# Kernel tuning notes

Measured on AMD Instinct MI355X. Metric: run time of the kernel, lower is better.

## Reference

```python
import jax, jax.numpy as jnp
import numpy as np

B, N, E = 2, 2048, 1024
H = 16
D = E // H  # head dim = 64


def setup_inputs() -> dict:
    key = jax.random.key(0)
    ks = jax.random.split(key, 11)
    s = 1.0 / np.sqrt(E)
    return {
        "q": jax.random.normal(ks[0], (B, N, E), jnp.float32),
        "k": jax.random.normal(ks[1], (B, N, E), jnp.float32),
        "v": jax.random.normal(ks[2], (B, N, E), jnp.float32),
        "Wq": jax.random.normal(ks[3], (E, E), jnp.float32) * s,
        "bq": jnp.zeros((E,), jnp.float32),
        "Wk": jax.random.normal(ks[4], (E, E), jnp.float32) * s,
        "bk": jnp.zeros((E,), jnp.float32),
        "Wv": jax.random.normal(ks[5], (E, E), jnp.float32) * s,
        "bv": jnp.zeros((E,), jnp.float32),
        "Wo": jax.random.normal(ks[6], (E, E), jnp.float32) * s,
        "bo": jnp.zeros((E,), jnp.float32),
    }


def reference(q, k, v, Wq, bq, Wk, bk, Wv, bv, Wo, bo):
    # projections (torch Linear: x @ W^T + b)
    qp = q @ Wq.T + bq  # [B,N,E]
    kp = k @ Wk.T + bk
    vp = v @ Wv.T + bv
    # separate heads -> [B,H,N,D]
    qh = qp.reshape(B, N, H, D).transpose(0, 2, 1, 3)
    kh = kp.reshape(B, N, H, D).transpose(0, 2, 1, 3)
    vh = vp.reshape(B, N, H, D).transpose(0, 2, 1, 3)
    # scaled dot-product attention, full score matrix like the original
    scale = 1.0 / jnp.sqrt(jnp.asarray(D, qh.dtype))
    attn = jnp.einsum('bhqd,bhkd->bhqk', qh, kh) * scale
    attn = jax.nn.softmax(attn, axis=-1)
    out = jnp.einsum('bhqk,bhkd->bhqd', attn, vh)  # [B,H,N,D]
    # recombine heads
    out = out.transpose(0, 2, 1, 3).reshape(B, N, E)
    return out @ Wo.T + bo
```

## Files before the change

kernel.cpp:

```cpp
#include <hip/hip_runtime.h>

typedef _Float16 f16;
typedef __attribute__((ext_vector_type(2))) _Float16 f16x2;
typedef __attribute__((ext_vector_type(4))) _Float16 f16x4;
typedef __attribute__((ext_vector_type(8))) _Float16 f16x8;
typedef __attribute__((ext_vector_type(4))) float    f32x4;
typedef __attribute__((ext_vector_type(16))) float   f32x16;
typedef __attribute__((ext_vector_type(4))) unsigned u32x4;

static constexpr int B_ = 2, N_ = 2048, E_ = 1024, H_ = 16, D_ = 64;
static constexpr int M_ = B_ * N_;

#define MFMA16(a, b, c) __builtin_amdgcn_mfma_f32_16x16x32_f16(a, b, c, 0, 0, 0)
#define MFMA32(a, b, c) __builtin_amdgcn_mfma_f32_32x32x16_f16(a, b, c, 0, 0, 0)

#define QSCALE 0.18033688011112042f

__device__ __forceinline__ void gload_lds16(const f16* g, f16* l) {
    typedef __attribute__((address_space(1))) const unsigned gu32;
    typedef __attribute__((address_space(3))) unsigned       lu32;
    __builtin_amdgcn_global_load_lds((gu32*)g, (lu32*)l, 16, 0, 0);
}

__global__ __launch_bounds__(256) void cast_all(
    const float* __restrict__ Wq, const float* __restrict__ Wk,
    const float* __restrict__ Wv, const float* __restrict__ Wo,
    const float* __restrict__ q, const float* __restrict__ k,
    const float* __restrict__ v, f16* __restrict__ dst)
{
    const int i = (blockIdx.x * 256 + threadIdx.x) * 4;
    const float* s;
    int j;
    if (i < 4 * E_ * E_) {
        const int which = i >> 20;
        s = (which == 0) ? Wq : (which == 1) ? Wk : (which == 2) ? Wv : Wo;
        j = i & (E_ * E_ - 1);
    } else {
        const int t = i - 4 * E_ * E_;
        const int which = t >> 22;
        s = (which == 0) ? q : (which == 1) ? k : v;
        j = t & (M_ * E_ - 1);
    }
    const f32x4 f = *(const f32x4*)&s[j];
    f16x4 o;
    o[0] = (f16)f[0]; o[1] = (f16)f[1]; o[2] = (f16)f[2]; o[3] = (f16)f[3];
    *(f16x4*)&dst[i] = o;
}

__global__ __launch_bounds__(256) void proj_gemm(
    const f16* __restrict__ Aall, const f16* __restrict__ Wb,
    const float* __restrict__ bq, const float* __restrict__ bk, const float* __restrict__ bv,
    f16* __restrict__ qh, f16* __restrict__ kh, f16* __restrict__ vt)
{
    const int bid  = blockIdx.x;
    const int lin  = (bid & 7) * 96 + (bid >> 3);
    const int z    = lin >> 8;
    const int rem  = lin & 255;
    const int m0   = (rem >> 3) * 128;
    const int n0   = (rem & 7) * 128;

    const f16* A    = Aall + (size_t)z * M_ * E_;
    const f16* W    = Wb + (size_t)z * E_ * E_;
    const float* bias = (z == 0) ? bq : (z == 1) ? bk : bv;

    __shared__ f16 As[128][32];
    __shared__ f16 Bs[128][32];

    const int tid  = threadIdx.x;
    const int lane = tid & 63, w = tid >> 6;
    const int lr = lane & 15, lg = lane >> 4;
    const int wm = (w >> 1) * 64, wn = (w & 1) * 64;

    const int gch = ((lane & 3) ^ ((lane >> 3) & 3)) * 8;
    const f16* ag = A + (size_t)(m0 + w * 32 + (lane >> 2)) * E_ + gch;
    const f16* bg = W + (size_t)(n0 + w * 32 + (lane >> 2)) * E_ + gch;
    f16* al0 = &As[w * 32][0];
    f16* al1 = &As[w * 32 + 16][0];
    f16* bl0 = &Bs[w * 32][0];
    f16* bl1 = &Bs[w * 32 + 16][0];

    const int ca = (lg ^ ((lr >> 1) & 3)) * 8;

    f32x4 acc[4][4];
#pragma unroll
    for (int i = 0; i < 4; i++)
#pragma unroll
        for (int j = 0; j < 4; j++) acc[i][j] = (f32x4){0.f, 0.f, 0.f, 0.f};

    for (int t = 0; t < E_ / 32; ++t) {
        __syncthreads();
        gload_lds16(ag,                 al0);
        gload_lds16(ag + 16 * E_,       al1);
        gload_lds16(bg,                 bl0);
        gload_lds16(bg + 16 * E_,       bl1);
        ag += 32; bg += 32;
        __syncthreads();

        f16x8 af[4], bfr[4];
#pragma unroll
        for (int ms = 0; ms < 4; ms++) af[ms]  = *(const f16x8*)&As[wm + ms * 16 + lr][ca];
#pragma unroll
        for (int ns = 0; ns < 4; ns++) bfr[ns] = *(const f16x8*)&Bs[wn + ns * 16 + lr][ca];
        __builtin_amdgcn_s_setprio(1);
#pragma unroll
        for (int ms = 0; ms < 4; ms++)
#pragma unroll
            for (int ns = 0; ns < 4; ns++)
                acc[ms][ns] = MFMA16(af[ms], bfr[ns], acc[ms][ns]);
        __builtin_amdgcn_s_setprio(0);
    }

    const float oscale = (z == 0) ? QSCALE : 1.0f;
#pragma unroll
    for (int ms = 0; ms < 4; ms++) {
        const int mbase = m0 + wm + ms * 16 + lg * 4;
#pragma unroll
        for (int ns = 0; ns < 4; ns++) {
            const int n  = n0 + wn + ns * 16 + lr;
            const float bn = bias[n];
            const int hh = n >> 6, dd = n & 63;
#pragma unroll
            for (int r = 0; r < 4; r++) {
                const float val = (acc[ms][ns][r] + bn) * oscale;
                const int mm = mbase + r;
                const int bb = mm >> 11;
                const int nn = mm & (N_ - 1);
                if (z == 2) {
                    vt[((size_t)(bb * H_ + hh) * D_ + dd) * N_ + nn] = (f16)val;
                } else {
                    f16* dst = (z == 0) ? qh : kh;
                    dst[((size_t)(bb * H_ + hh) * N_ + nn) * D_ + dd] = (f16)val;
                }
            }
        }
    }
}

__global__ __launch_bounds__(256) void attn_kernel(
    const f16* __restrict__ qh, const f16* __restrict__ kh,
    const f16* __restrict__ vt, f16* __restrict__ ao)
{
    const int bid = blockIdx.x;
    const int swz = (bid & 7) * 64 + (bid >> 3);
    const int qt = swz & 15;
    const int bh = swz >> 4;

    const int tid = threadIdx.x;
    const int w = tid >> 6, lane = tid & 63;
    const int l31 = lane & 31;
    const bool hi = (lane >> 5) != 0;
    const int hib = hi ? 1 : 0;

    const f16* qp = qh + (size_t)bh * N_ * D_;
    const f16* kp = kh + (size_t)bh * N_ * D_;
    const f16* vp = vt + (size_t)bh * D_ * N_;

    const int qrow = qt * 128 + w * 32 + l31;

    f16x8 qf[4];
#pragma unroll
    for (int ks = 0; ks < 4; ks++)
        qf[ks] = *(const f16x8*)&qp[(size_t)qrow * D_ + ks * 16 + hib * 8];

    __shared__ f16 Ks[2][64][64];
    __shared__ f16 Vs[2][64][64];

    const int srow = tid >> 3;
    const int sch  = tid & 7;
    const int ssl  = (sch ^ (srow & 7)) * 8;

    const f16* kg0 = kp + (size_t)srow * D_ + sch * 8;
    const f16* kg1 = kg0 + (size_t)32 * D_;
    const f16* vg0 = vp + (size_t)srow * N_ + sch * 8;
    const f16* vg1 = vg0 + (size_t)32 * N_;

    f32x16 oT0 = {0.f,0.f,0.f,0.f,0.f,0.f,0.f,0.f,0.f,0.f,0.f,0.f,0.f,0.f,0.f,0.f};
    f32x16 oT1 = oT0;
    float mrun = -3.0e38f, lrun = 0.f;

    f16x8 kr0 = *(const f16x8*)(kg0);
    f16x8 kr1 = *(const f16x8*)(kg1);
    f16x8 vr0 = *(const f16x8*)(vg0);
    f16x8 vr1 = *(const f16x8*)(vg1);

    constexpr int NT = N_ / 64;
    int cur = 0;

    for (int t = 0; t < NT; ++t) {
        *(f16x8*)&Ks[cur][srow     ][ssl] = kr0;
        *(f16x8*)&Ks[cur][srow + 32][ssl] = kr1;
        *(f16x8*)&Vs[cur][srow     ][ssl] = vr0;
        *(f16x8*)&Vs[cur][srow + 32][ssl] = vr1;
        if (t + 1 < NT) {
            kr0 = *(const f16x8*)(kg0 + (size_t)(t + 1) * 64 * D_);
            kr1 = *(const f16x8*)(kg1 + (size_t)(t + 1) * 64 * D_);
            vr0 = *(const f16x8*)(vg0 + (t + 1) * 64);
            vr1 = *(const f16x8*)(vg1 + (t + 1) * 64);
        }
        __syncthreads();

        f32x16 sA = {0.f,0.f,0.f,0.f,0.f,0.f,0.f,0.f,0.f,0.f,0.f,0.f,0.f,0.f,0.f,0.f};
        f32x16 sB = sA;
        __builtin_amdgcn_s_setprio(1);
#pragma unroll
        for (int ks = 0; ks < 4; ks++) {
            const int c = (ks * 2 + hib) ^ (l31 & 7);
            const f16x8 kfA = *(const f16x8*)&Ks[cur][l31     ][c * 8];
            const f16x8 kfB = *(const f16x8*)&Ks[cur][l31 + 32][c * 8];
            sA = MFMA32(kfA, qf[ks], sA);
            sB = MFMA32(kfB, qf[ks], sB);
        }
        __builtin_amdgcn_s_setprio(0);

        float tt[16];
#pragma unroll
        for (int r = 0; r < 16; r++) tt[r] = fmaxf(sA[r], sB[r]);
#pragma unroll
        for (int d = 8; d >= 1; d >>= 1)
#pragma unroll
            for (int r = 0; r < d; r++) tt[r] = fmaxf(tt[r], tt[r + d]);
        float pmax = fmaxf(tt[0], __shfl_xor(tt[0], 32));

        if (!__all(pmax - mrun <= 8.0f)) {
            const float mnew = fmaxf(mrun, pmax);
            const float alpha = __builtin_amdgcn_exp2f(mrun - mnew);
            mrun = mnew;
            lrun *= alpha;
#pragma unroll
            for (int r = 0; r < 16; r++) { oT0[r] *= alpha; oT1[r] *= alpha; }
        }

        float p0 = 0.f, p1 = 0.f, p2 = 0.f, p3 = 0.f;
#pragma unroll
        for (int r = 0; r < 16; r += 4) {
            sA[r]   = __builtin_amdgcn_exp2f(sA[r]   - mrun); p0 += sA[r];
            sA[r+1] = __builtin_amdgcn_exp2f(sA[r+1] - mrun); p1 += sA[r+1];
            sA[r+2] = __builtin_amdgcn_exp2f(sA[r+2] - mrun); p2 += sA[r+2];
            sA[r+3] = __builtin_amdgcn_exp2f(sA[r+3] - mrun); p3 += sA[r+3];
        }
#pragma unroll
        for (int r = 0; r < 16; r += 4) {
            sB[r]   = __builtin_amdgcn_exp2f(sB[r]   - mrun); p0 += sB[r];
            sB[r+1] = __builtin_amdgcn_exp2f(sB[r+1] - mrun); p1 += sB[r+1];
            sB[r+2] = __builtin_amdgcn_exp2f(sB[r+2] - mrun); p2 += sB[r+2];
            sB[r+3] = __builtin_amdgcn_exp2f(sB[r+3] - mrun); p3 += sB[r+3];
        }
        float lsum = (p0 + p1) + (p2 + p3);
        lsum += __shfl_xor(lsum, 32);
        lrun += lsum;

        __builtin_amdgcn_s_setprio(1);
#define PVSTEP(PP0,PP1,PP2,PP3,PP4,PP5,PP6,PP7, KSI)                                   \
        {                                                                              \
            const unsigned w0 = __builtin_bit_cast(unsigned, __builtin_amdgcn_cvt_pkrtz(PP0, PP1)); \
            const unsigned w1 = __builtin_bit_cast(unsigned, __builtin_amdgcn_cvt_pkrtz(PP2, PP3)); \
            const unsigned w2 = __builtin_bit_cast(unsigned, __builtin_amdgcn_cvt_pkrtz(PP4, PP5)); \
            const unsigned w3 = __builtin_bit_cast(unsigned, __builtin_amdgcn_cvt_pkrtz(PP6, PP7)); \
            const unsigned x0 = (unsigned)__shfl_xor((int)w0, 32);                     \
            const unsigned x1 = (unsigned)__shfl_xor((int)w1, 32);                     \
            const unsigned x2 = (unsigned)__shfl_xor((int)w2, 32);                     \
            const unsigned x3 = (unsigned)__shfl_xor((int)w3, 32);                     \
            u32x4 pw;                                                                  \
            pw[0] = hi ? x2 : w0;                                                      \
            pw[1] = hi ? x3 : w1;                                                      \
            pw[2] = hi ? w2 : x0;                                                      \
            pw[3] = hi ? w3 : x1;                                                      \
            const f16x8 pa = __builtin_bit_cast(f16x8, pw);                            \
            const int c = ((KSI) * 2 + hib) ^ (l31 & 7);                               \
            const f16x8 vf0 = *(const f16x8*)&Vs[cur][l31     ][c * 8];                \
            const f16x8 vf1 = *(const f16x8*)&Vs[cur][l31 + 32][c * 8];                \
            oT0 = MFMA32(vf0, pa, oT0);                                                \
            oT1 = MFMA32(vf1, pa, oT1);                                                \
        }
        PVSTEP(sA[0],sA[1],sA[2],sA[3],sA[4],sA[5],sA[6],sA[7], 0)
        PVSTEP(sA[8],sA[9],sA[10],sA[11],sA[12],sA[13],sA[14],sA[15], 1)
        PVSTEP(sB[0],sB[1],sB[2],sB[3],sB[4],sB[5],sB[6],sB[7], 2)
        PVSTEP(sB[8],sB[9],sB[10],sB[11],sB[12],sB[13],sB[14],sB[15], 3)
#undef PVSTEP
        __builtin_amdgcn_s_setprio(0);

        cur ^= 1;
    }

    const float inv = 1.0f / lrun;
    const int b = bh >> 4, h = bh & 15;
    f16* dst = ao + (size_t)(b * N_ + qrow) * E_ + h * 64 + hib * 4;
#pragma unroll
    for (int g = 0; g < 4; g++) {
        f16x4 o0, o1;
#pragma unroll
        for (int j = 0; j < 4; j++) {
            o0[j] = (f16)(oT0[g * 4 + j] * inv);
            o1[j] = (f16)(oT1[g * 4 + j] * inv);
        }
        *(f16x4*)&dst[8 * g]      = o0;
        *(f16x4*)&dst[8 * g + 32] = o1;
    }
}

__global__ __launch_bounds__(256) void out_gemm(
    const f16* __restrict__ ao, const f16* __restrict__ Wo,
    const float* __restrict__ bo, float* __restrict__ out)
{
    __shared__ f16 As[128][32];
    __shared__ f16 Bs[128][32];

    const int bid = blockIdx.x;
    const int lin = (bid & 7) * 32 + (bid >> 3);
    const int m0  = (lin >> 3) * 128;
    const int n0  = (lin & 7) * 128;

    const int tid  = threadIdx.x;
    const int lane = tid & 63, w = tid >> 6;
    const int lr = lane & 15, lg = lane >> 4;
    const int wm = (w >> 1) * 64, wn = (w & 1) * 64;

    const int gch = ((lane & 3) ^ ((lane >> 3) & 3)) * 8;
    const f16* ag = ao + (size_t)(m0 + w * 32 + (lane >> 2)) * E_ + gch;
    const f16* bg = Wo + (size_t)(n0 + w * 32 + (lane >> 2)) * E_ + gch;
    f16* al0 = &As[w * 32][0];
    f16* al1 = &As[w * 32 + 16][0];
    f16* bl0 = &Bs[w * 32][0];
    f16* bl1 = &Bs[w * 32 + 16][0];

    const int ca = (lg ^ ((lr >> 1) & 3)) * 8;

    f32x4 acc[4][4];
#pragma unroll
    for (int i = 0; i < 4; i++)
#pragma unroll
        for (int j = 0; j < 4; j++) acc[i][j] = (f32x4){0.f, 0.f, 0.f, 0.f};

    for (int t = 0; t < E_ / 32; ++t) {
        __syncthreads();
        gload_lds16(ag,            al0);
        gload_lds16(ag + 16 * E_,  al1);
        gload_lds16(bg,            bl0);
        gload_lds16(bg + 16 * E_,  bl1);
        ag += 32; bg += 32;
        __syncthreads();

        f16x8 af[4], bfr[4];
#pragma unroll
        for (int ms = 0; ms < 4; ms++) af[ms]  = *(const f16x8*)&As[wm + ms * 16 + lr][ca];
#pragma unroll
        for (int ns = 0; ns < 4; ns++) bfr[ns] = *(const f16x8*)&Bs[wn + ns * 16 + lr][ca];
        __builtin_amdgcn_s_setprio(1);
#pragma unroll
        for (int ms = 0; ms < 4; ms++)
#pragma unroll
            for (int ns = 0; ns < 4; ns++)
                acc[ms][ns] = MFMA16(af[ms], bfr[ns], acc[ms][ns]);
        __builtin_amdgcn_s_setprio(0);
    }

#pragma unroll
    for (int ms = 0; ms < 4; ms++) {
        const int mbase = m0 + wm + ms * 16 + lg * 4;
#pragma unroll
        for (int ns = 0; ns < 4; ns++) {
            const int n = n0 + wn + ns * 16 + lr;
            const float bn = bo[n];
#pragma unroll
            for (int r = 0; r < 4; r++) {
                out[(size_t)(mbase + r) * E_ + n] = acc[ms][ns][r] + bn;
            }
        }
    }
}

extern "C" void kernel_launch(void* const* d_in, const int* in_sizes, int n_in,
                              void* d_out, int out_size, void* d_ws, size_t ws_size,
                              hipStream_t stream) {
    const float* q  = (const float*)d_in[0];
    const float* k  = (const float*)d_in[1];
    const float* v  = (const float*)d_in[2];
    const float* Wq = (const float*)d_in[3];
    const float* bq = (const float*)d_in[4];
    const float* Wk = (const float*)d_in[5];
    const float* bk = (const float*)d_in[6];
    const float* Wv = (const float*)d_in[7];
    const float* bv = (const float*)d_in[8];
    const float* Wo = (const float*)d_in[9];
    const float* bo = (const float*)d_in[10];
    float* out = (float*)d_out;

    char* ws = (char*)d_ws;
    f16* cast = (f16*)ws;
    f16* Wb   = cast;
    f16* Aall = cast + (size_t)4 * E_ * E_;
    f16* qh = (f16*)(ws + (size_t)32 * 1024 * 1024);
    f16* kh = (f16*)(ws + (size_t)40 * 1024 * 1024);
    f16* vt = (f16*)(ws + (size_t)48 * 1024 * 1024);
    f16* ao = (f16*)(ws + (size_t)56 * 1024 * 1024);

    cast_all<<<16384, 256, 0, stream>>>(Wq, Wk, Wv, Wo, q, k, v, cast);
    proj_gemm<<<768, 256, 0, stream>>>(Aall, Wb, bq, bk, bv, qh, kh, vt);
    attn_kernel<<<512, 256, 0, stream>>>(qh, kh, vt, ao);
    out_gemm<<<256, 256, 0, stream>>>(ao, Wb + (size_t)3 * E_ * E_, bo, out);
}
```

Baseline: 149.7 us.

## Split attention KV range across wave pairs and load K/V via direct-to-LDS

The attention kernel now uses 64-query tiles with two wave groups each processing half of the KV sequence, then merges the partial softmax states through shared memory. The launch doubles to 1024 blocks with a 4-waves-per-SIMD occupancy hint. K/V tiles are fetched with global_load_lds, so the projection GEMM pre-swizzles its K and V output layouts to match the LDS bank-conflict-avoiding pattern. The KV loads are no longer register-prefetched or double-buffered across iterations, which may expose load latency, and the final merge adds a sync plus shared-memory traffic.

```diff
diff --git a/kernel.cpp b/kernel.cpp
--- a/kernel.cpp
+++ b/kernel.cpp
@@ -89,10 +89,10 @@
 
     for (int t = 0; t < E_ / 32; ++t) {
         __syncthreads();
-        gload_lds16(ag,                 al0);
-        gload_lds16(ag + 16 * E_,       al1);
-        gload_lds16(bg,                 bl0);
-        gload_lds16(bg + 16 * E_,       bl1);
+        gload_lds16(ag,            al0);
+        gload_lds16(ag + 16 * E_,  al1);
+        gload_lds16(bg,            bl0);
+        gload_lds16(bg + 16 * E_,  bl1);
         ag += 32; bg += 32;
         __syncthreads();
 
@@ -125,28 +125,32 @@
                 const int mm = mbase + r;
                 const int bb = mm >> 11;
                 const int nn = mm & (N_ - 1);
-                if (z == 2) {
-                    vt[((size_t)(bb * H_ + hh) * D_ + dd) * N_ + nn] = (f16)val;
+                if (z == 0) {
+                    qh[((size_t)(bb * H_ + hh) * N_ + nn) * D_ + dd] = (f16)val;
+                } else if (z == 1) {
+                    const int ddsw = ((((dd >> 3) ^ nn) & 7) << 3) | (dd & 7);
+                    kh[((size_t)(bb * H_ + hh) * N_ + nn) * D_ + ddsw] = (f16)val;
                 } else {
-                    f16* dst = (z == 0) ? qh : kh;
-                    dst[((size_t)(bb * H_ + hh) * N_ + nn) * D_ + dd] = (f16)val;
+                    const int nnsw = (nn & ~63) | ((((nn >> 3) ^ dd) & 7) << 3) | (nn & 7);
+                    vt[((size_t)(bb * H_ + hh) * D_ + dd) * N_ + nnsw] = (f16)val;
                 }
             }
         }
     }
 }
 
-__global__ __launch_bounds__(256) void attn_kernel(
+__global__ __launch_bounds__(256, 4) void attn_kernel(
     const f16* __restrict__ qh, const f16* __restrict__ kh,
     const f16* __restrict__ vt, f16* __restrict__ ao)
 {
     const int bid = blockIdx.x;
-    const int swz = (bid & 7) * 64 + (bid >> 3);
-    const int qt = swz & 15;
-    const int bh = swz >> 4;
+    const int swz = (bid & 7) * 128 + (bid >> 3);
+    const int qt = swz & 31;
+    const int bh = swz >> 5;
 
     const int tid = threadIdx.x;
     const int w = tid >> 6, lane = tid & 63;
+    const int qg = w & 1, kvg = w >> 1;
     const int l31 = lane & 31;
     const bool hi = (lane >> 5) != 0;
     const int hib = hi ? 1 : 0;
@@ -155,47 +159,32 @@
     const f16* kp = kh + (size_t)bh * N_ * D_;
     const f16* vp = vt + (size_t)bh * D_ * N_;
 
-    const int qrow = qt * 128 + w * 32 + l31;
+    const int qrow = qt * 64 + qg * 32 + l31;
 
     f16x8 qf[4];
 #pragma unroll
     for (int ks = 0; ks < 4; ks++)
         qf[ks] = *(const f16x8*)&qp[(size_t)qrow * D_ + ks * 16 + hib * 8];
 
-    __shared__ f16 Ks[2][64][64];
-    __shared__ f16 Vs[2][64][64];
-
-    const int srow = tid >> 3;
-    const int sch  = tid & 7;
-    const int ssl  = (sch ^ (srow & 7)) * 8;
-
-    const f16* kg0 = kp + (size_t)srow * D_ + sch * 8;
-    const f16* kg1 = kg0 + (size_t)32 * D_;
-    const f16* vg0 = vp + (size_t)srow * N_ + sch * 8;
-    const f16* vg1 = vg0 + (size_t)32 * N_;
+    __shared__ union SmemU {
+        struct { f16 K[2][64][64]; f16 V[2][64][64]; } s;
+        float M[2][64][34];
+    } sm;
+
+    const int srB = qg * 32 + (lane >> 3);
+    const f16* kgb = kp + ((size_t)(kvg * 16 * 64 + srB)) * 64 + (lane & 7) * 8;
+    const f16* vgb = vp + (size_t)srB * N_ + kvg * 16 * 64 + (lane & 7) * 8;
 
     f32x16 oT0 = {0.f,0.f,0.f,0.f,0.f,0.f,0.f,0.f,0.f,0.f,0.f,0.f,0.f,0.f,0.f,0.f};
     f32x16 oT1 = oT0;
     float mrun = -3.0e38f, lrun = 0.f;
 
-    f16x8 kr0 = *(const f16x8*)(kg0);
-    f16x8 kr1 = *(const f16x8*)(kg1);
-    f16x8 vr0 = *(const f16x8*)(vg0);
-    f16x8 vr1 = *(const f16x8*)(vg1);
-
-    constexpr int NT = N_ / 64;
-    int cur = 0;
-
-    for (int t = 0; t < NT; ++t) {
-        *(f16x8*)&Ks[cur][srow     ][ssl] = kr0;
-        *(f16x8*)&Ks[cur][srow + 32][ssl] = kr1;
-        *(f16x8*)&Vs[cur][srow     ][ssl] = vr0;
-        *(f16x8*)&Vs[cur][srow + 32][ssl] = vr1;
-        if (t + 1 < NT) {
-            kr0 = *(const f16x8*)(kg0 + (size_t)(t + 1) * 64 * D_);
-            kr1 = *(const f16x8*)(kg1 + (size_t)(t + 1) * 64 * D_);
-            vr0 = *(const f16x8*)(vg0 + (t + 1) * 64);
-            vr1 = *(const f16x8*)(vg1 + (t + 1) * 64);
+    for (int t = 0; t < 16; ++t) {
+        __syncthreads();
+#pragma unroll
+        for (int i = 0; i < 4; i++) {
+            gload_lds16(kgb + (size_t)t * 4096 + i * 512, &sm.s.K[kvg][qg * 32 + i * 8][0]);
+            gload_lds16(vgb + t * 64 + (size_t)i * 8 * N_, &sm.s.V[kvg][qg * 32 + i * 8][0]);
         }
         __syncthreads();
 
@@ -205,21 +194,25 @@
 #pragma unroll
         for (int ks = 0; ks < 4; ks++) {
             const int c = (ks * 2 + hib) ^ (l31 & 7);
-            const f16x8 kfA = *(const f16x8*)&Ks[cur][l31     ][c * 8];
-            const f16x8 kfB = *(const f16x8*)&Ks[cur][l31 + 32][c * 8];
+            const f16x8 kfA = *(const f16x8*)&sm.s.K[kvg][l31     ][c * 8];
+            const f16x8 kfB = *(const f16x8*)&sm.s.K[kvg][l31 + 32][c * 8];
             sA = MFMA32(kfA, qf[ks], sA);
             sB = MFMA32(kfB, qf[ks], sB);
         }
         __builtin_amdgcn_s_setprio(0);
 
-        float tt[16];
-#pragma unroll
-        for (int r = 0; r < 16; r++) tt[r] = fmaxf(sA[r], sB[r]);
-#pragma unroll
-        for (int d = 8; d >= 1; d >>= 1)
-#pragma unroll
-            for (int r = 0; r < d; r++) tt[r] = fmaxf(tt[r], tt[r + d]);
-        float pmax = fmaxf(tt[0], __shfl_xor(tt[0], 32));
+        float t16[16];
+#pragma unroll
+        for (int r = 0; r < 16; r++) t16[r] = fmaxf(sA[r], sB[r]);
+        const float u0 = fmaxf(fmaxf(t16[0],  t16[1]),  t16[2]);
+        const float u1 = fmaxf(fmaxf(t16[3],  t16[4]),  t16[5]);
+        const float u2 = fmaxf(fmaxf(t16[6],  t16[7]),  t16[8]);
+        const float u3 = fmaxf(fmaxf(t16[9],  t16[10]), t16[11]);
+        const float u4 = fmaxf(fmaxf(t16[12], t16[13]), t16[14]);
+        const float v0 = fmaxf(fmaxf(u0, u1), u2);
+        const float v1 = fmaxf(fmaxf(u3, u4), t16[15]);
+        const float tmax = fmaxf(v0, v1);
+        const float pmax = fmaxf(tmax, __shfl_xor(tmax, 32));
 
         if (!__all(pmax - mrun <= 8.0f)) {
             const float mnew = fmaxf(mrun, pmax);
@@ -267,8 +260,8 @@
             pw[3] = hi ? w3 : x1;                                                      \
             const f16x8 pa = __builtin_bit_cast(f16x8, pw);                            \
             const int c = ((KSI) * 2 + hib) ^ (l31 & 7);                               \
-            const f16x8 vf0 = *(const f16x8*)&Vs[cur][l31     ][c * 8];                \
-            const f16x8 vf1 = *(const f16x8*)&Vs[cur][l31 + 32][c * 8];                \
+            const f16x8 vf0 = *(const f16x8*)&sm.s.V[kvg][l31     ][c * 8];            \
+            const f16x8 vf1 = *(const f16x8*)&sm.s.V[kvg][l31 + 32][c * 8];            \
             oT0 = MFMA32(vf0, pa, oT0);                                                \
             oT1 = MFMA32(vf1, pa, oT1);                                                \
         }
@@ -278,23 +271,36 @@
         PVSTEP(sB[8],sB[9],sB[10],sB[11],sB[12],sB[13],sB[14],sB[15], 3)
 #undef PVSTEP
         __builtin_amdgcn_s_setprio(0);
-
-        cur ^= 1;
-    }
-
-    const float inv = 1.0f / lrun;
-    const int b = bh >> 4, h = bh & 15;
-    f16* dst = ao + (size_t)(b * N_ + qrow) * E_ + h * 64 + hib * 4;
-#pragma unroll
-    for (int g = 0; g < 4; g++) {
-        f16x4 o0, o1;
-#pragma unroll
-        for (int j = 0; j < 4; j++) {
-            o0[j] = (f16)(oT0[g * 4 + j] * inv);
-            o1[j] = (f16)(oT1[g * 4 + j] * inv);
-        }
-        *(f16x4*)&dst[8 * g]      = o0;
-        *(f16x4*)&dst[8 * g + 32] = o1;
+    }
+
+    __syncthreads();
+    if (kvg == 1) {
+        float* Mq = &sm.M[qg][lane][0];
+#pragma unroll
+        for (int r = 0; r < 16; r++) { Mq[r] = oT0[r]; Mq[16 + r] = oT1[r]; }
+        Mq[32] = mrun; Mq[33] = lrun;
+    }
+    __syncthreads();
+    if (kvg == 0) {
+        const float* Mq = &sm.M[qg][lane][0];
+        const float pm = Mq[32], pl = Mq[33];
+        const float m  = fmaxf(mrun, pm);
+        const float a1 = __builtin_amdgcn_exp2f(mrun - m);
+        const float a2 = __builtin_amdgcn_exp2f(pm - m);
+        const float inv = 1.0f / (lrun * a1 + pl * a2);
+        const int b = bh >> 4, h = bh & 15;
+        f16* dst = ao + (size_t)(b * N_ + qrow) * E_ + h * 64 + hib * 4;
+#pragma unroll
+        for (int g = 0; g < 4; g++) {
+            f16x4 o0, o1;
+#pragma unroll
+            for (int j = 0; j < 4; j++) {
+                o0[j] = (f16)((oT0[g * 4 + j] * a1 + Mq[g * 4 + j]      * a2) * inv);
+                o1[j] = (f16)((oT1[g * 4 + j] * a1 + Mq[16 + g * 4 + j] * a2) * inv);
+            }
+            *(f16x4*)&dst[8 * g]      = o0;
+            *(f16x4*)&dst[8 * g + 32] = o1;
+        }
     }
 }
 
@@ -396,6 +402,6 @@
 
     cast_all<<<16384, 256, 0, stream>>>(Wq, Wk, Wv, Wo, q, k, v, cast);
     proj_gemm<<<768, 256, 0, stream>>>(Aall, Wb, bq, bk, bv, qh, kh, vt);
-    attn_kernel<<<512, 256, 0, stream>>>(qh, kh, vt, ao);
+    attn_kernel<<<1024, 256, 0, stream>>>(qh, kh, vt, ao);
     out_gemm<<<256, 256, 0, stream>>>(ao, Wb + (size_t)3 * E_ * E_, bo, out);
 }
```

After: 173.6 us. +16.0%, slower.

## Shrink attention blocks to two waves with 64-row query tiles, doubling grid

Applied to the files above, without the earlier changes.

Attention blocks now use 128 threads (two wavefronts) that cover 64 query rows instead of 128, and the grid grows from 512 to 1024 blocks. Each thread therefore stages four K and four V row chunks per tile instead of two. The row max reduction is also rewritten as a flatter tree of three-input fmaxf calls, meant to map onto v_max3. The aim is more blocks for better CU occupancy and load balance, at the cost of each K/V tile being loaded once per 64 query rows, which doubles K/V traffic.

```diff
diff --git a/kernel.cpp b/kernel.cpp
--- a/kernel.cpp
+++ b/kernel.cpp
@@ -89,10 +89,10 @@
 
     for (int t = 0; t < E_ / 32; ++t) {
         __syncthreads();
-        gload_lds16(ag,                 al0);
-        gload_lds16(ag + 16 * E_,       al1);
-        gload_lds16(bg,                 bl0);
-        gload_lds16(bg + 16 * E_,       bl1);
+        gload_lds16(ag,            al0);
+        gload_lds16(ag + 16 * E_,  al1);
+        gload_lds16(bg,            bl0);
+        gload_lds16(bg + 16 * E_,  bl1);
         ag += 32; bg += 32;
         __syncthreads();
 
@@ -136,14 +136,14 @@
     }
 }
 
-__global__ __launch_bounds__(256) void attn_kernel(
+__global__ __launch_bounds__(128) void attn_kernel(
     const f16* __restrict__ qh, const f16* __restrict__ kh,
     const f16* __restrict__ vt, f16* __restrict__ ao)
 {
     const int bid = blockIdx.x;
-    const int swz = (bid & 7) * 64 + (bid >> 3);
-    const int qt = swz & 15;
-    const int bh = swz >> 4;
+    const int swz = (bid & 7) * 128 + (bid >> 3);
+    const int qt = swz & 31;
+    const int bh = swz >> 5;
 
     const int tid = threadIdx.x;
     const int w = tid >> 6, lane = tid & 63;
@@ -155,7 +155,7 @@
     const f16* kp = kh + (size_t)bh * N_ * D_;
     const f16* vp = vt + (size_t)bh * D_ * N_;
 
-    const int qrow = qt * 128 + w * 32 + l31;
+    const int qrow = qt * 64 + w * 32 + l31;
 
     f16x8 qf[4];
 #pragma unroll
@@ -169,33 +169,35 @@
     const int sch  = tid & 7;
     const int ssl  = (sch ^ (srow & 7)) * 8;
 
-    const f16* kg0 = kp + (size_t)srow * D_ + sch * 8;
-    const f16* kg1 = kg0 + (size_t)32 * D_;
-    const f16* vg0 = vp + (size_t)srow * N_ + sch * 8;
-    const f16* vg1 = vg0 + (size_t)32 * N_;
+    const f16* kg = kp + (size_t)srow * D_ + sch * 8;
+    const f16* vg = vp + (size_t)srow * N_ + sch * 8;
 
     f32x16 oT0 = {0.f,0.f,0.f,0.f,0.f,0.f,0.f,0.f,0.f,0.f,0.f,0.f,0.f,0.f,0.f,0.f};
     f32x16 oT1 = oT0;
     float mrun = -3.0e38f, lrun = 0.f;
 
-    f16x8 kr0 = *(const f16x8*)(kg0);
-    f16x8 kr1 = *(const f16x8*)(kg1);
-    f16x8 vr0 = *(const f16x8*)(vg0);
-    f16x8 vr1 = *(const f16x8*)(vg1);
+    f16x8 kreg[4], vreg[4];
+#pragma unroll
+    for (int i = 0; i < 4; i++) {
+        kreg[i] = *(const f16x8*)(kg + (size_t)i * 16 * D_);
+        vreg[i] = *(const f16x8*)(vg + (size_t)i * 16 * N_);
+    }
 
     constexpr int NT = N_ / 64;
     int cur = 0;
 
     for (int t = 0; t < NT; ++t) {
-        *(f16x8*)&Ks[cur][srow     ][ssl] = kr0;
-        *(f16x8*)&Ks[cur][srow + 32][ssl] = kr1;
-        *(f16x8*)&Vs[cur][srow     ][ssl] = vr0;
-        *(f16x8*)&Vs[cur][srow + 32][ssl] = vr1;
+#pragma unroll
+        for (int i = 0; i < 4; i++) {
+            *(f16x8*)&Ks[cur][srow + 16 * i][ssl] = kreg[i];
+            *(f16x8*)&Vs[cur][srow + 16 * i][ssl] = vreg[i];
+        }
         if (t + 1 < NT) {
-            kr0 = *(const f16x8*)(kg0 + (size_t)(t + 1) * 64 * D_);
-            kr1 = *(const f16x8*)(kg1 + (size_t)(t + 1) * 64 * D_);
-            vr0 = *(const f16x8*)(vg0 + (t + 1) * 64);
-            vr1 = *(const f16x8*)(vg1 + (t + 1) * 64);
+#pragma unroll
+            for (int i = 0; i < 4; i++) {
+                kreg[i] = *(const f16x8*)(kg + (size_t)(t + 1) * 64 * D_ + (size_t)i * 16 * D_);
+                vreg[i] = *(const f16x8*)(vg + (t + 1) * 64 + (size_t)i * 16 * N_);
+            }
         }
         __syncthreads();
 
@@ -212,14 +214,18 @@
         }
         __builtin_amdgcn_s_setprio(0);
 
-        float tt[16];
-#pragma unroll
-        for (int r = 0; r < 16; r++) tt[r] = fmaxf(sA[r], sB[r]);
-#pragma unroll
-        for (int d = 8; d >= 1; d >>= 1)
-#pragma unroll
-            for (int r = 0; r < d; r++) tt[r] = fmaxf(tt[r], tt[r + d]);
-        float pmax = fmaxf(tt[0], __shfl_xor(tt[0], 32));
+        float t16[16];
+#pragma unroll
+        for (int r = 0; r < 16; r++) t16[r] = fmaxf(sA[r], sB[r]);
+        const float u0 = fmaxf(fmaxf(t16[0],  t16[1]),  t16[2]);
+        const float u1 = fmaxf(fmaxf(t16[3],  t16[4]),  t16[5]);
+        const float u2 = fmaxf(fmaxf(t16[6],  t16[7]),  t16[8]);
+        const float u3 = fmaxf(fmaxf(t16[9],  t16[10]), t16[11]);
+        const float u4 = fmaxf(fmaxf(t16[12], t16[13]), t16[14]);
+        const float v0 = fmaxf(fmaxf(u0, u1), u2);
+        const float v1 = fmaxf(fmaxf(u3, u4), t16[15]);
+        const float tmax = fmaxf(v0, v1);
+        const float pmax = fmaxf(tmax, __shfl_xor(tmax, 32));
 
         if (!__all(pmax - mrun <= 8.0f)) {
             const float mnew = fmaxf(mrun, pmax);
@@ -396,6 +402,6 @@
 
     cast_all<<<16384, 256, 0, stream>>>(Wq, Wk, Wv, Wo, q, k, v, cast);
     proj_gemm<<<768, 256, 0, stream>>>(Aall, Wb, bq, bk, bv, qh, kh, vt);
-    attn_kernel<<<512, 256, 0, stream>>>(qh, kh, vt, ao);
+    attn_kernel<<<1024, 128, 0, stream>>>(qh, kh, vt, ao);
     out_gemm<<<256, 256, 0, stream>>>(ao, Wb + (size_t)3 * E_ * E_, bo, out);
 }
```

Measured after the change: 156.3 us. 4.4% more time.

## Split attention over two KV halves and merge partial outputs

Applied to the files above, without the earlier changes.

The attention kernel now splits each (batch, head, query-tile) into two blocks, each covering half of the keys. Each block writes an unnormalised-then-normalised partial output plus its running max and sum. A new merge kernel combines the two halves with log-sum-exp weights into the head-interleaved layout. The aim is to double the grid from 512 to 1024 blocks for better CU occupancy and latency hiding, at the cost of an extra kernel launch and extra global traffic for the partial outputs and statistics.

```diff
diff --git a/kernel.cpp b/kernel.cpp
--- a/kernel.cpp
+++ b/kernel.cpp
@@ -89,10 +89,10 @@
 
     for (int t = 0; t < E_ / 32; ++t) {
         __syncthreads();
-        gload_lds16(ag,                 al0);
-        gload_lds16(ag + 16 * E_,       al1);
-        gload_lds16(bg,                 bl0);
-        gload_lds16(bg + 16 * E_,       bl1);
+        gload_lds16(ag,            al0);
+        gload_lds16(ag + 16 * E_,  al1);
+        gload_lds16(bg,            bl0);
+        gload_lds16(bg + 16 * E_,  bl1);
         ag += 32; bg += 32;
         __syncthreads();
 
@@ -138,12 +138,14 @@
 
 __global__ __launch_bounds__(256) void attn_kernel(
     const f16* __restrict__ qh, const f16* __restrict__ kh,
-    const f16* __restrict__ vt, f16* __restrict__ ao)
+    const f16* __restrict__ vt, f16* __restrict__ Op, float* __restrict__ ml)
 {
     const int bid = blockIdx.x;
-    const int swz = (bid & 7) * 64 + (bid >> 3);
-    const int qt = swz & 15;
-    const int bh = swz >> 4;
+    const int lin = (bid & 7) * 128 + (bid >> 3);
+    const int bh  = lin >> 5;
+    const int rem = lin & 31;
+    const int qt  = rem >> 1;
+    const int kvh = rem & 1;
 
     const int tid = threadIdx.x;
     const int w = tid >> 6, lane = tid & 63;
@@ -152,8 +154,8 @@
     const int hib = hi ? 1 : 0;
 
     const f16* qp = qh + (size_t)bh * N_ * D_;
-    const f16* kp = kh + (size_t)bh * N_ * D_;
-    const f16* vp = vt + (size_t)bh * D_ * N_;
+    const f16* kp = kh + ((size_t)bh * N_ + kvh * 1024) * D_;
+    const f16* vp = vt + (size_t)bh * D_ * N_ + kvh * 1024;
 
     const int qrow = qt * 128 + w * 32 + l31;
 
@@ -183,7 +185,7 @@
     f16x8 vr0 = *(const f16x8*)(vg0);
     f16x8 vr1 = *(const f16x8*)(vg1);
 
-    constexpr int NT = N_ / 64;
+    constexpr int NT = 1024 / 64;
     int cur = 0;
 
     for (int t = 0; t < NT; ++t) {
@@ -212,14 +214,14 @@
         }
         __builtin_amdgcn_s_setprio(0);
 
-        float tt[16];
-#pragma unroll
-        for (int r = 0; r < 16; r++) tt[r] = fmaxf(sA[r], sB[r]);
+        float t16[16];
+#pragma unroll
+        for (int r = 0; r < 16; r++) t16[r] = fmaxf(sA[r], sB[r]);
 #pragma unroll
         for (int d = 8; d >= 1; d >>= 1)
 #pragma unroll
-            for (int r = 0; r < d; r++) tt[r] = fmaxf(tt[r], tt[r + d]);
-        float pmax = fmaxf(tt[0], __shfl_xor(tt[0], 32));
+            for (int r = 0; r < d; r++) t16[r] = fmaxf(t16[r], t16[r + d]);
+        const float pmax = fmaxf(t16[0], __shfl_xor(t16[0], 32));
 
         if (!__all(pmax - mrun <= 8.0f)) {
             const float mnew = fmaxf(mrun, pmax);
@@ -283,8 +285,8 @@
     }
 
     const float inv = 1.0f / lrun;
-    const int b = bh >> 4, h = bh & 15;
-    f16* dst = ao + (size_t)(b * N_ + qrow) * E_ + h * 64 + hib * 4;
+    const size_t prow = ((size_t)(kvh * 32 + bh) * N_ + qrow);
+    f16* dst = Op + prow * D_ + hib * 4;
 #pragma unroll
     for (int g = 0; g < 4; g++) {
         f16x4 o0, o1;
@@ -296,6 +298,41 @@
         *(f16x4*)&dst[8 * g]      = o0;
         *(f16x4*)&dst[8 * g + 32] = o1;
     }
+    if (!hi) {
+        ml[prow * 2]     = mrun;
+        ml[prow * 2 + 1] = lrun;
+    }
+}
+
+__global__ __launch_bounds__(256) void attn_merge(
+    const f16* __restrict__ Op, const float* __restrict__ ml,
+    f16* __restrict__ ao)
+{
+    const int t  = blockIdx.x * 256 + threadIdx.x;
+    const int d8 = t & 7;
+    const int qr = (t >> 3) & (N_ - 1);
+    const int bh = t >> 14;
+
+    const size_t r0 = (size_t)bh * N_ + qr;
+    const size_t r1 = (size_t)(32 + bh) * N_ + qr;
+
+    const float m0 = ml[r0 * 2], l0 = ml[r0 * 2 + 1];
+    const float m1 = ml[r1 * 2], l1 = ml[r1 * 2 + 1];
+    const float m  = fmaxf(m0, m1);
+    const float w0 = l0 * __builtin_amdgcn_exp2f(m0 - m);
+    const float w1 = l1 * __builtin_amdgcn_exp2f(m1 - m);
+    const float s0 = w0 / (w0 + w1);
+    const float s1 = 1.0f - s0;
+
+    const f16x8 o0 = *(const f16x8*)&Op[r0 * D_ + d8 * 8];
+    const f16x8 o1 = *(const f16x8*)&Op[r1 * D_ + d8 * 8];
+    f16x8 o;
+#pragma unroll
+    for (int j = 0; j < 8; j++)
+        o[j] = (f16)(s0 * (float)o0[j] + s1 * (float)o1[j]);
+
+    const int b = bh >> 4, h = bh & 15;
+    *(f16x8*)&ao[((size_t)(b * N_ + qr)) * E_ + h * 64 + d8 * 8] = o;
 }
 
 __global__ __launch_bounds__(256) void out_gemm(
@@ -393,9 +430,12 @@
     f16* kh = (f16*)(ws + (size_t)40 * 1024 * 1024);
     f16* vt = (f16*)(ws + (size_t)48 * 1024 * 1024);
     f16* ao = (f16*)(ws + (size_t)56 * 1024 * 1024);
+    f16*   Op = (f16*)(ws + (size_t)8 * 1024 * 1024);
+    float* ml = (float*)(ws + (size_t)24 * 1024 * 1024);
 
     cast_all<<<16384, 256, 0, stream>>>(Wq, Wk, Wv, Wo, q, k, v, cast);
     proj_gemm<<<768, 256, 0, stream>>>(Aall, Wb, bq, bk, bv, qh, kh, vt);
-    attn_kernel<<<512, 256, 0, stream>>>(qh, kh, vt, ao);
+    attn_kernel<<<1024, 256, 0, stream>>>(qh, kh, vt, Op, ml);
+    attn_merge<<<2048, 256, 0, stream>>>(Op, ml, ao);
     out_gemm<<<256, 256, 0, stream>>>(ao, Wb + (size_t)3 * E_ * E_, bo, out);
 }
```

Result: slower. 155.9 us (+4.1%).
